# Optimization experiments

Hardware: AMD Instinct MI355X
Metric: run time of the kernel (lower is better)

## Reference

```python
import jax, jax.numpy as jnp
import numpy as np

N, E, D, ED, G = 50000, 800000, 64, 32, 50


def setup_inputs() -> dict:
    key = jax.random.key(0)
    ks = jax.random.split(key, 24)
    s = 0.05
    inp = {
        "x": jax.random.normal(ks[0], (N, D), jnp.float32),
        "edge_attr": jax.random.normal(ks[1], (E, ED), jnp.float32),
        "edge_index": jax.random.randint(ks[2], (2, E), 0, N, jnp.int64),
    }
    i = 3
    for step in range(2):
        inp[f"fe{step}_W1"] = jax.random.normal(ks[i], (2 * D + ED, D), jnp.float32) * s; i += 1
        inp[f"fe{step}_b1"] = jnp.zeros((D,), jnp.float32)
        inp[f"fe{step}_W2"] = jax.random.normal(ks[i], (D, D), jnp.float32) * s; i += 1
        inp[f"fe{step}_b2"] = jnp.zeros((D,), jnp.float32)
        inp[f"lstm{step}_Wih"] = jax.random.normal(ks[i], (D, 4 * D), jnp.float32) * s; i += 1
        inp[f"lstm{step}_Whh"] = jax.random.normal(ks[i], (D, 4 * D), jnp.float32) * s; i += 1
        inp[f"lstm{step}_bih"] = jnp.zeros((4 * D,), jnp.float32)
        inp[f"lstm{step}_bhh"] = jnp.zeros((4 * D,), jnp.float32)
    inp["gm_W"] = jax.random.normal(ks[i], (D, G), jnp.float32) * s; i += 1
    inp["gm_b"] = jnp.zeros((G,), jnp.float32)
    inp["fm_W"] = jax.random.normal(ks[i], (D, G), jnp.float32) * s; i += 1
    inp["fm_b"] = jnp.zeros((G,), jnp.float32)
    return inp


def _mpn(x, edge_attr, src, dst, W1, b1, W2, b2):
    # x_i = x[dst] (target), x_j = x[src] (source); aggregate 'add' at dst
    m = jnp.concatenate([x[dst], x[src], edge_attr], axis=1)  # [E, 2D+ED]
    m = jax.nn.relu(m @ W1 + b1) @ W2 + b2                    # [E, D]
    return jax.ops.segment_sum(m, dst, num_segments=x.shape[0])


def _lstm_cell(inp, h, c, Wih, Whh, bih, bhh):
    gates = inp @ Wih + h @ Whh + (bih + bhh)  # [N, 4D], gate order i,f,g,o
    i, f, g, o = jnp.split(gates, 4, axis=1)
    c = jax.nn.sigmoid(f) * c + jax.nn.sigmoid(i) * jnp.tanh(g)
    h = jax.nn.sigmoid(o) * jnp.tanh(c)
    return h, c


def reference(x, edge_attr, edge_index,
              fe0_W1, fe0_b1, fe0_W2, fe0_b2,
              lstm0_Wih, lstm0_Whh, lstm0_bih, lstm0_bhh,
              fe1_W1, fe1_b1, fe1_W2, fe1_b2,
              lstm1_Wih, lstm1_Whh, lstm1_bih, lstm1_bhh,
              gm_W, gm_b, fm_W, fm_b):
    src, dst = edge_index[0], edge_index[1]
    c = jnp.zeros_like(x)
    fes = [(fe0_W1, fe0_b1, fe0_W2, fe0_b2), (fe1_W1, fe1_b1, fe1_W2, fe1_b2)]
    lstms = [(lstm0_Wih, lstm0_Whh, lstm0_bih, lstm0_bhh),
             (lstm1_Wih, lstm1_Whh, lstm1_bih, lstm1_bhh)]
    for step in range(2):
        a = _mpn(x, edge_attr, src, dst, *fes[step])
        # LSTMCell(input=x, (h=a, c=c)) as in the original forward
        x, c = _lstm_cell(x, a, c, *lstms[step])
    g = jax.nn.sigmoid(x @ gm_W + gm_b)   # [N, G]
    h_v_G = x @ fm_W + fm_b               # [N, G]
    return jnp.sum(g * h_v_G, axis=0)     # [G]
```

## Files before the change

### kernel.cpp

```cpp
#include <hip/hip_runtime.h>
#include <hip/hip_bf16.h>

using short8 = __attribute__((ext_vector_type(8))) short;
using f32x4  = __attribute__((ext_vector_type(4))) float;

#define KLP 136

__device__ __forceinline__ unsigned short f2bf(float f) {
  unsigned u = __float_as_uint(f);
  u += 0x7FFFu + ((u >> 16) & 1u);
  return (unsigned short)(u >> 16);
}
__device__ __forceinline__ unsigned pack2(float a, float b) {
  return (unsigned)f2bf(a) | ((unsigned)f2bf(b) << 16);
}
#if __has_builtin(__builtin_amdgcn_rcpf)
__device__ __forceinline__ float fast_rcp(float x) { return __builtin_amdgcn_rcpf(x); }
#else
__device__ __forceinline__ float fast_rcp(float x) { return 1.f / x; }
#endif
__device__ __forceinline__ float sigm(float x) { return fast_rcp(1.f + __expf(-x)); }
__device__ __forceinline__ float tanh_f(float x) { return fmaf(2.f, sigm(2.f * x), -1.f); }

__global__ __launch_bounds__(256) void prep_all(
    const float* __restrict__ x,
    const float* __restrict__ W1_0, const float* __restrict__ Wih0,
    const float* __restrict__ bih0, const float* __restrict__ bhh0,
    const float* __restrict__ W1_1, const float* __restrict__ Wih1,
    const float* __restrict__ bih1, const float* __restrict__ bhh1,
    const float* __restrict__ W2_0, const float* __restrict__ Whh0, const float* __restrict__ b2_0,
    const float* __restrict__ W2_1, const float* __restrict__ Whh1, const float* __restrict__ b2_1,
    const float* __restrict__ gmW, const float* __restrict__ fmW,
    unsigned short* __restrict__ W1T,
    unsigned short* __restrict__ WcT,
    float* __restrict__ bG,
    float* __restrict__ b2h,
    unsigned short* __restrict__ WrT,
    unsigned short* __restrict__ xb0,
    float* __restrict__ aggrH,
    int* __restrict__ histA,
    float* __restrict__ outZ, int nOut,
    int N)
{
  int t = blockIdx.x * 256 + threadIdx.x;

  const int R0 = 2 * 26880 + 8192;
  if (t < R0) {
    const int per = 26880;
    if (t >= 2 * per) {
      int r2 = t - 2 * per;
      int o = r2 >> 6, k = r2 & 63;
      float v = 0.f;
      if (o < 50) v = gmW[k * 50 + o];
      else if (o >= 64 && o < 114) v = fmW[k * 50 + (o - 64)];
      WrT[o * 64 + k] = f2bf(v);
      return;
    }
    int step = t / per, r = t % per;
    const float* W1  = step ? W1_1 : W1_0;
    const float* Wih = step ? Wih1 : Wih0;
    const float* bih = step ? bih1 : bih0;
    const float* bhh = step ? bhh1 : bhh0;
    if (r < 10240) {
      int o = r / 160, k = r % 160;
      W1T[step * 10240 + o * 160 + k] = f2bf(W1[k * 64 + o]);
    } else if (r < 26624) {
      int rr = r - 10240;
      int g = rr >> 6, k = rr & 63;
      WcT[step * 32768 + g * 128 + k] = f2bf(Wih[k * 256 + g]);
    } else {
      int g = r - 26624;
      bG[step * 256 + g] = bih[g] + bhh[g];
    }
    return;
  }
  t -= R0;

  const int R1 = 33280;
  if (t < R1) {
    if (t < 32768) {
      int step = t >> 14, r = t & 16383;
      int g = r >> 6, k = r & 63;
      const float* W2  = step ? W2_1 : W2_0;
      const float* Whh = step ? Whh1 : Whh0;
      float v = 0.f;
      for (int j = 0; j < 64; ++j) v = fmaf(W2[k * 64 + j], Whh[j * 256 + g], v);
      WcT[step * 32768 + g * 128 + 64 + k] = f2bf(v);
    } else {
      int r = t - 32768;
      int step = r >> 8, g = r & 255;
      const float* b2  = step ? b2_1 : b2_0;
      const float* Whh = step ? Whh1 : Whh0;
      float v = 0.f;
      for (int j = 0; j < 64; ++j) v = fmaf(b2[j], Whh[j * 256 + g], v);
      b2h[step * 256 + g] = v;
    }
    return;
  }
  t -= R1;

  const int R2 = N * 8;
  if (t < R2) {
    const float4* p = (const float4*)(x + (long long)t * 8);
    float4 a0 = p[0], a1 = p[1];
    *(uint4*)(xb0 + (long long)t * 8) =
        make_uint4(pack2(a0.x, a0.y), pack2(a0.z, a0.w), pack2(a1.x, a1.y), pack2(a1.z, a1.w));
    return;
  }
  t -= R2;

  const int R3 = N * 16;
  if (t < R3) { ((float4*)aggrH)[t] = make_float4(0.f, 0.f, 0.f, 0.f); return; }
  t -= R3;

  const int R4 = N / 4;
  if (t < R4) { ((int4*)histA)[t] = make_int4(0, 0, 0, 0); return; }
  t -= R4;

  if (t < nOut) outZ[t] = 0.f;
}

__global__ __launch_bounds__(256) void hist_kernel(
    const int* __restrict__ dstI, int* __restrict__ hist, int E)
{
  int e = blockIdx.x * 256 + threadIdx.x;
  if (e < E) atomicAdd(&hist[dstI[e]], 1);
}

__global__ __launch_bounds__(256) void scan_part(
    const int* __restrict__ hist, int2* __restrict__ blockTot, int N)
{
  __shared__ int sD[256], sS[256];
  int t = threadIdx.x;
  int n = blockIdx.x * 256 + t;
  int d = (n < N) ? hist[n] : 0;
  int sg = (d + 15) >> 4;
  sD[t] = d; sS[t] = sg;
  __syncthreads();
  #pragma unroll
  for (int off = 128; off; off >>= 1) {
    if (t < off) { sD[t] += sD[t + off]; sS[t] += sS[t + off]; }
    __syncthreads();
  }
  if (t == 0) blockTot[blockIdx.x] = make_int2(sD[0], sS[0]);
}

__global__ __launch_bounds__(256) void scan_mid(
    const int2* __restrict__ blockTot, int2* __restrict__ blockBase,
    int* __restrict__ nSegTot, int nb)
{
  __shared__ int sD[256], sS[256];
  int t = threadIdx.x;
  int d = 0, s = 0;
  if (t < nb) { int2 v = blockTot[t]; d = v.x; s = v.y; }
  sD[t] = d; sS[t] = s;
  __syncthreads();
  #pragma unroll
  for (int off = 1; off < 256; off <<= 1) {
    int vd = (t >= off) ? sD[t - off] : 0;
    int vs = (t >= off) ? sS[t - off] : 0;
    __syncthreads();
    sD[t] += vd; sS[t] += vs;
    __syncthreads();
  }
  if (t < nb) blockBase[t] = make_int2(sD[t] - d, sS[t] - s);
  if (t == nb - 1) *nSegTot = sS[t];
}

__global__ __launch_bounds__(256) void scan_final(
    const int* __restrict__ hist, const int2* __restrict__ blockBase,
    int* __restrict__ cursor, int4* __restrict__ segInfo, int N)
{
  __shared__ int sD[256], sS[256];
  int t = threadIdx.x;
  int n = blockIdx.x * 256 + t;
  int d = (n < N) ? hist[n] : 0;
  int sg = (d + 15) >> 4;
  sD[t] = d; sS[t] = sg;
  __syncthreads();
  #pragma unroll
  for (int off = 1; off < 256; off <<= 1) {
    int vd = (t >= off) ? sD[t - off] : 0;
    int vs = (t >= off) ? sS[t - off] : 0;
    __syncthreads();
    sD[t] += vd; sS[t] += vs;
    __syncthreads();
  }
  if (n < N) {
    int2 bb = blockBase[blockIdx.x];
    int degBase = bb.x + sD[t] - d;
    int segBase = bb.y + sS[t] - sg;
    cursor[n] = degBase;
    for (int j = 0; j < sg; ++j)
      segInfo[segBase + j] = make_int4(degBase + j * 16, n, min(d - j * 16, 16), 0);
  }
}

__global__ __launch_bounds__(256) void scatter_perm(
    const int* __restrict__ srcI, const int* __restrict__ dstI,
    const float* __restrict__ ea, int* __restrict__ cursor,
    int* __restrict__ srcS, unsigned short* __restrict__ eaS, int E)
{
  const int t = threadIdx.x;
  const int l = t & 63;
  const int e = blockIdx.x * 64 + (t >> 2);
  const int c = t & 3;
  if (e >= E) return;
  int p = 0;
  if (c == 0) {
    int d = dstI[e];
    p = atomicAdd(&cursor[d], 1);
    srcS[p] = srcI[e];
  }
  p = __shfl(p, l & ~3);
  const float4* pe = (const float4*)(ea + (long long)e * 32 + c * 8);
  float4 a0 = pe[0], a1 = pe[1];
  *(uint4*)(eaS + (long long)p * 32 + c * 8) =
      make_uint4(pack2(a0.x, a0.y), pack2(a0.z, a0.w), pack2(a1.x, a1.y), pack2(a1.z, a1.w));
}

__global__ __launch_bounds__(256) void dst_gemm(
    const unsigned short* __restrict__ xb,
    const unsigned short* __restrict__ W1T,
    const float* __restrict__ b1,
    float* __restrict__ D,
    int nNodes)
{
  __shared__ unsigned short sX[64 * 72];
  const int t = threadIdx.x;
  const int base = blockIdx.x * 64;
  const int nl = t >> 2, q = t & 3;
  const int node = base + nl;
  {
    uint4* dst = (uint4*)(sX + nl * 72 + q * 16);
    if (node < nNodes) {
      const uint4* px = (const uint4*)(xb + (long long)node * 64);
      dst[0] = px[q * 2];
      dst[1] = px[q * 2 + 1];
    } else {
      dst[0] = make_uint4(0, 0, 0, 0);
      dst[1] = make_uint4(0, 0, 0, 0);
    }
  }
  const int w = t >> 6, l = t & 63, quad = l >> 4, lr = l & 15;
  short8 bF[2][4];
  #pragma unroll
  for (int kc = 0; kc < 2; ++kc)
    #pragma unroll
    for (int n = 0; n < 4; ++n)
      bF[kc][n] = *(const short8*)(W1T + (n * 16 + lr) * 160 + kc * 32 + quad * 8);
  float bb[4];
  #pragma unroll
  for (int n = 0; n < 4; ++n) bb[n] = b1[n * 16 + lr];
  __syncthreads();

  f32x4 acc[4] = {};
  #pragma unroll
  for (int kc = 0; kc < 2; ++kc) {
    short8 aF = *(const short8*)(sX + (w * 16 + lr) * 72 + kc * 32 + quad * 8);
    #pragma unroll
    for (int n = 0; n < 4; ++n)
      acc[n] = __builtin_amdgcn_mfma_f32_16x16x32_bf16(aF, bF[kc][n], acc[n], 0, 0, 0);
  }
  #pragma unroll
  for (int n = 0; n < 4; ++n) {
    #pragma unroll
    for (int rr = 0; rr < 4; ++rr) {
      int nd = base + w * 16 + quad * 4 + rr;
      if (nd < nNodes)
        D[(long long)nd * 64 + n * 16 + lr] = acc[n][rr] + bb[n];
    }
  }
}

__global__ __launch_bounds__(256) void edge_gemm(
    const unsigned short* __restrict__ xb,
    const unsigned short* __restrict__ eaS,
    const int* __restrict__ srcS,
    const int4* __restrict__ segInfo,
    const int* __restrict__ nSegPtr,
    const unsigned short* __restrict__ W1T,
    const float* __restrict__ D,
    float* __restrict__ aggrH)
{
  __shared__ unsigned short stash[12 * 64 * 8];
  const int t = threadIdx.x;
  const int w = t >> 6, l = t & 63;
  const int quad = l >> 4, lr = l & 15;

  #pragma unroll
  for (int p = 0; p < 3; ++p) {
    int idx = p * 256 + t;
    int grp = idx >> 6, ll = idx & 63;
    int kc = 2 + (grp >> 2), n = grp & 3;
    *(uint4*)(stash + idx * 8) =
        *(const uint4*)(W1T + (n * 16 + (ll & 15)) * 160 + kc * 32 + (ll >> 4) * 8);
  }
  __syncthreads();

  const int nSeg = *nSegPtr;
  const int W = gridDim.x * 4;
  int s = blockIdx.x * 4 + w;
  if (s >= nSeg) return;

  int4 si = segInfo[s];
  short8 A2, A3, A4;
  float Dv0, Dv1, Dv2, Dv3;
  {
    int src0 = srcS[si.x + min(lr, si.z - 1)];
    const short8* ps = (const short8*)(xb + (long long)src0 * 64);
    A2 = ps[quad];
    A3 = ps[4 + quad];
    A4 = *(const short8*)(eaS + (long long)(si.x + min(lr, si.z - 1)) * 32 + quad * 8);
    const float* dp = D + (long long)si.y * 64 + lr;
    Dv0 = dp[0]; Dv1 = dp[16]; Dv2 = dp[32]; Dv3 = dp[48];
  }
  int sn = s + W;
  bool more = sn < nSeg;
  int4 si_n = si;
  int src_n = 0;
  if (more) {
    si_n = segInfo[sn];
    src_n = srcS[si_n.x + min(lr, si_n.z - 1)];
  }

  while (true) {
    short8 B2 = A2, B3 = A3, B4 = A4;
    float En0 = Dv0, En1 = Dv1, En2 = Dv2, En3 = Dv3;
    if (more) {
      const short8* ps = (const short8*)(xb + (long long)src_n * 64);
      B2 = ps[quad];
      B3 = ps[4 + quad];
      B4 = *(const short8*)(eaS + (long long)(si_n.x + min(lr, si_n.z - 1)) * 32 + quad * 8);
      const float* dp = D + (long long)si_n.y * 64 + lr;
      En0 = dp[0]; En1 = dp[16]; En2 = dp[32]; En3 = dp[48];
    }
    int snn = sn + W;
    bool more2 = more && (snn < nSeg);
    int4 si_nn = si_n;
    int src_nn = src_n;
    if (more2) {
      si_nn = segInfo[snn];
      src_nn = srcS[si_nn.x + min(lr, si_nn.z - 1)];
    }

    const int node = si.y, cnt = si.z;
    f32x4 acc[4] = {};
    #pragma unroll
    for (int kc = 0; kc < 3; ++kc) {
      short8 aX = (kc == 0) ? A2 : (kc == 1) ? A3 : A4;
      #pragma unroll
      for (int n = 0; n < 4; ++n) {
        short8 bFr = *(const short8*)(stash + (((kc << 2) | n) * 64 + l) * 8);
        acc[n] = __builtin_amdgcn_mfma_f32_16x16x32_bf16(aX, bFr, acc[n], 0, 0, 0);
      }
    }

    float myv = 0.f;
    #pragma unroll
    for (int n = 0; n < 4; ++n) {
      float bias = (n == 0) ? Dv0 : (n == 1) ? Dv1 : (n == 2) ? Dv2 : Dv3;
      float sum = 0.f;
      #pragma unroll
      for (int rr = 0; rr < 4; ++rr) {
        float v = fmaxf(acc[n][rr] + bias, 0.f);
        sum += (quad * 4 + rr < cnt) ? v : 0.f;
      }
      sum += __shfl_xor(sum, 16);
      sum += __shfl_xor(sum, 32);
      if (quad == n) myv = sum;
    }
    unsafeAtomicAdd(&aggrH[(long long)node * 64 + l], myv);

    if (!more) break;
    si = si_n; A2 = B2; A3 = B3; A4 = B4;
    Dv0 = En0; Dv1 = En1; Dv2 = En2; Dv3 = En3;
    sn = snn; si_n = si_nn; src_n = src_nn; more = more2;
  }
}

__global__ __launch_bounds__(256) void lstm3(
    const unsigned short* __restrict__ xbin,
    float* __restrict__ aggrH,
    const float* __restrict__ cin,
    float* __restrict__ cout,
    const unsigned short* __restrict__ WcT,
    const float* __restrict__ bG,
    const float* __restrict__ b2h,
    const int* __restrict__ degA,
    unsigned short* __restrict__ xbout,
    const unsigned short* __restrict__ WrT,
    const float* __restrict__ gb, const float* __restrict__ fb,
    float* __restrict__ outG,
    int nNodes, int zeroAggr, int doReadout)
{
  __shared__ unsigned short sIn[64 * KLP];
  __shared__ unsigned short sW[128 * 72];
  __shared__ float sBG[256], sB2h[256];
  const int t = threadIdx.x;
  sBG[t] = bG[t];
  sB2h[t] = b2h[t];

  const int base_n = blockIdx.x * 64;
  const int nl = t >> 2, q = t & 3;
  const int node = base_n + nl;
  unsigned short* rowp = sIn + nl * KLP;
  if (node < nNodes) {
    const uint4* px = (const uint4*)(xbin + (long long)node * 64);
    *(uint4*)(rowp + q * 16)     = px[q * 2];
    *(uint4*)(rowp + q * 16 + 8) = px[q * 2 + 1];
    float4* pg = (float4*)(aggrH + (long long)node * 64) + q * 4;
    float4 g0 = pg[0], g1 = pg[1], g2 = pg[2], g3 = pg[3];
    *(uint4*)(rowp + 64 + q * 16) =
        make_uint4(pack2(g0.x, g0.y), pack2(g0.z, g0.w), pack2(g1.x, g1.y), pack2(g1.z, g1.w));
    *(uint4*)(rowp + 64 + q * 16 + 8) =
        make_uint4(pack2(g2.x, g2.y), pack2(g2.z, g2.w), pack2(g3.x, g3.y), pack2(g3.z, g3.w));
    if (zeroAggr) {
      float4 z = make_float4(0.f, 0.f, 0.f, 0.f);
      pg[0] = z; pg[1] = z; pg[2] = z; pg[3] = z;
    }
  } else {
    *(uint4*)(rowp + q * 16)          = make_uint4(0, 0, 0, 0);
    *(uint4*)(rowp + q * 16 + 8)      = make_uint4(0, 0, 0, 0);
    *(uint4*)(rowp + 64 + q * 16)     = make_uint4(0, 0, 0, 0);
    *(uint4*)(rowp + 64 + q * 16 + 8) = make_uint4(0, 0, 0, 0);
  }

  const int w = t >> 6, l = t & 63, quad = l >> 4, lr = l & 15;
  const int row0 = w * 16;
  f32x4 acc[16] = {};
  for (int grp = 0; grp < 4; ++grp) {
    const uint4* gw = (const uint4*)WcT + (long long)(grp * 64) * 16;
    uint4* lw = (uint4*)sW;
    {
      int o0 = t >> 4, s4 = t & 15;
      #pragma unroll
      for (int pp = 0; pp < 4; ++pp) {
        int o = pp * 16 + o0;
        lw[o * 17 + s4] = gw[o * 16 + s4];
      }
    }
    __syncthreads();
    #pragma unroll
    for (int kc = 0; kc < 4; ++kc) {
      short8 aF = *(const short8*)(sIn + (row0 + lr) * KLP + kc * 32 + quad * 8);
      #pragma unroll
      for (int nt = 0; nt < 4; ++nt) {
        short8 bF = *(const short8*)(sW + (nt * 16 + lr) * KLP + kc * 32 + quad * 8);
        acc[grp * 4 + nt] = __builtin_amdgcn_mfma_f32_16x16x32_bf16(aF, bF, acc[grp * 4 + nt], 0, 0, 0);
      }
    }
    __syncthreads();
  }

  #pragma unroll
  for (int nt = 0; nt < 4; ++nt) {
    #pragma unroll
    for (int rr = 0; rr < 4; ++rr) {
      int node2 = base_n + row0 + quad * 4 + rr;
      int rl = row0 + quad * 4 + rr;
      int col = nt * 16 + lr;
      if (node2 < nNodes) {
        long long off = (long long)node2 * 64 + col;
        float dg = (float)degA[node2];
        float iv = acc[nt][rr]      + sBG[col]       + dg * sB2h[col];
        float fv = acc[4 + nt][rr]  + sBG[64 + col]  + dg * sB2h[64 + col];
        float gv = acc[8 + nt][rr]  + sBG[128 + col] + dg * sB2h[128 + col];
        float ov = acc[12 + nt][rr] + sBG[192 + col] + dg * sB2h[192 + col];
        float cOld = cin ? cin[off] : 0.f;
        float cN = sigm(fv) * cOld + sigm(iv) * tanh_f(gv);
        float hN = sigm(ov) * tanh_f(cN);
        if (doReadout) {
          sIn[rl * 72 + col] = f2bf(hN);
        } else {
          cout[off] = cN;
          xbout[off] = f2bf(hN);
        }
      } else if (doReadout) {
        sIn[rl * 72 + col] = 0;
      }
    }
  }

  if (!doReadout) return;

  __syncthreads();
  {
    const uint4* gw = (const uint4*)WrT;
    uint4* lw = (uint4*)sW;
    #pragma unroll
    for (int pp = 0; pp < 4; ++pp) {
      int idx = t + pp * 256;
      int o = idx >> 3, s = idx & 7;
      lw[o * 9 + s] = gw[idx];
    }
  }
  if (t < 64) {
    sBG[t]      = (t < 50) ? gb[t] : 0.f;
    sBG[64 + t] = (t < 50) ? fb[t] : 0.f;
  }
  __syncthreads();

  f32x4 racc[8] = {};
  #pragma unroll
  for (int kc = 0; kc < 2; ++kc) {
    short8 aF = *(const short8*)(sIn + (w * 16 + lr) * 72 + kc * 32 + quad * 8);
    #pragma unroll
    for (int n = 0; n < 8; ++n) {
      short8 bF = *(const short8*)(sW + (n * 16 + lr) * 72 + kc * 32 + quad * 8);
      racc[n] = __builtin_amdgcn_mfma_f32_16x16x32_bf16(aF, bF, racc[n], 0, 0, 0);
    }
  }
  float* sOutF = sB2h;
  #pragma unroll
  for (int n = 0; n < 4; ++n) {
    float val = 0.f;
    #pragma unroll
    for (int rr = 0; rr < 4; ++rr) {
      int nd = base_n + w * 16 + quad * 4 + rr;
      if (nd < nNodes) {
        int jj = n * 16 + lr;
        float gv = sigm(racc[n][rr] + sBG[jj]);
        float fv = racc[n + 4][rr] + sBG[64 + jj];
        val += gv * fv;
      }
    }
    val += __shfl_xor(val, 16);
    val += __shfl_xor(val, 32);
    if (quad == 0) sOutF[w * 64 + n * 16 + lr] = val;
  }
  __syncthreads();
  if (t < 50) {
    float sm = sOutF[t] + sOutF[64 + t] + sOutF[128 + t] + sOutF[192 + t];
    unsafeAtomicAdd(&outG[t], sm);
  }
}

extern "C" void kernel_launch(void* const* d_in, const int* in_sizes, int n_in,
                              void* d_out, int out_size, void* d_ws, size_t ws_size,
                              hipStream_t stream)
{
  const float* x      = (const float*)d_in[0];
  const float* ea     = (const float*)d_in[1];
  const int*   ei     = (const int*)d_in[2];
  const float* fe0_W1 = (const float*)d_in[3];
  const float* fe0_b1 = (const float*)d_in[4];
  const float* fe0_W2 = (const float*)d_in[5];
  const float* fe0_b2 = (const float*)d_in[6];
  const float* l0_Wih = (const float*)d_in[7];
  const float* l0_Whh = (const float*)d_in[8];
  const float* l0_bih = (const float*)d_in[9];
  const float* l0_bhh = (const float*)d_in[10];
  const float* fe1_W1 = (const float*)d_in[11];
  const float* fe1_b1 = (const float*)d_in[12];
  const float* fe1_W2 = (const float*)d_in[13];
  const float* fe1_b2 = (const float*)d_in[14];
  const float* l1_Wih = (const float*)d_in[15];
  const float* l1_Whh = (const float*)d_in[16];
  const float* l1_bih = (const float*)d_in[17];
  const float* l1_bhh = (const float*)d_in[18];
  const float* gm_W   = (const float*)d_in[19];
  const float* gm_b   = (const float*)d_in[20];
  const float* fm_W   = (const float*)d_in[21];
  const float* fm_b   = (const float*)d_in[22];

  const int N = in_sizes[0] / 64;
  const int E = in_sizes[1] / 32;
  const int* srcI = ei;
  const int* dstI = ei + E;

  char* ws = (char*)d_ws;
  unsigned short* xb0     = (unsigned short*)(ws + 0);
  unsigned short* xb1     = (unsigned short*)(ws + 6400000);
  float*          aggrH   = (float*)(ws + 12800000);
  float*          cbuf    = (float*)(ws + 25600000);
  unsigned short* eaS     = (unsigned short*)(ws + 38400000);
  int*            srcS    = (int*)(ws + 89601024);
  int4*           segInfo = (int4*)(ws + 92801088);
  int*            histA   = (int*)(ws + 94401280);
  int*            curA    = (int*)(ws + 94601280);
  unsigned short* W1T     = (unsigned short*)(ws + 94801280);
  unsigned short* WcT     = (unsigned short*)(ws + 94842240);
  float*          bG      = (float*)(ws + 94973312);
  float*          b2h     = (float*)(ws + 94975360);
  unsigned short* WrT     = (unsigned short*)(ws + 94977408);
  int*            nSegPtr = (int*)(ws + 94993792);
  int2*           blockTot  = (int2*)(ws + 94993856);
  int2*           blockBase = (int2*)(ws + 94995904);
  float*          Dbuf    = (float*)(ws + 96000000);

  const int prepT = (2 * 26880 + 8192) + 33280 + N * 8 + N * 16 + N / 4 + out_size;
  prep_all<<<(prepT + 255) / 256, 256, 0, stream>>>(
      x,
      fe0_W1, l0_Wih, l0_bih, l0_bhh,
      fe1_W1, l1_Wih, l1_bih, l1_bhh,
      fe0_W2, l0_Whh, fe0_b2,
      fe1_W2, l1_Whh, fe1_b2,
      gm_W, fm_W,
      W1T, WcT, bG, b2h, WrT, xb0,
      aggrH, histA, (float*)d_out, out_size, N);

  const int nb = (N + 255) / 256;
  hist_kernel<<<(E + 255) / 256, 256, 0, stream>>>(dstI, histA, E);
  scan_part<<<nb, 256, 0, stream>>>(histA, blockTot, N);
  scan_mid<<<1, 256, 0, stream>>>(blockTot, blockBase, nSegPtr, nb);
  scan_final<<<nb, 256, 0, stream>>>(histA, blockBase, curA, segInfo, N);
  scatter_perm<<<(E + 63) / 64, 256, 0, stream>>>(srcI, dstI, ea, curA, srcS, eaS, E);

  const int nodeBlocks = (N + 63) / 64;

  dst_gemm<<<nodeBlocks, 256, 0, stream>>>(xb0, W1T, fe0_b1, Dbuf, N);
  edge_gemm<<<2048, 256, 0, stream>>>(xb0, eaS, srcS, segInfo, nSegPtr,
                                      W1T, Dbuf, aggrH);
  lstm3<<<nodeBlocks, 256, 0, stream>>>(xb0, aggrH, nullptr, cbuf, WcT, bG, b2h,
                                        histA, xb1, WrT, gm_b, fm_b, (float*)d_out,
                                        N, 1, 0);

  dst_gemm<<<nodeBlocks, 256, 0, stream>>>(xb1, W1T + 10240, fe1_b1, Dbuf, N);
  edge_gemm<<<2048, 256, 0, stream>>>(xb1, eaS, srcS, segInfo, nSegPtr,
                                      W1T + 10240, Dbuf, aggrH);
  lstm3<<<nodeBlocks, 256, 0, stream>>>(xb1, aggrH, cbuf, nullptr, WcT + 32768,
                                        bG + 256, b2h + 256, histA, nullptr,
                                        WrT, gm_b, fm_b, (float*)d_out,
                                        N, 0, 1);
}
```

Measured before the change: 423.9 us.

## Fuse step-1 dst GEMM into LSTM and give edge_gemm contiguous segment ranges

The first LSTM kernel now also computes the next message-passing step's destination-projection term (h @ W1 dst slice + b1) from the staged hidden state in LDS. This removes a separate dst_gemm launch and its re-read of xb1. Separately, edge_gemm warps now process a contiguous chunk of segments rather than a grid-strided set. Consecutive segments of the same node are summed in registers and flushed with a single atomic, which cuts global atomics. Contiguous chunking can unbalance work across warps and shortens the prefetch distance from two segments to one.

```diff
diff --git a/kernel.cpp b/kernel.cpp
--- a/kernel.cpp
+++ b/kernel.cpp
@@ -299,49 +299,42 @@
   __syncthreads();
 
   const int nSeg = *nSegPtr;
-  const int W = gridDim.x * 4;
-  int s = blockIdx.x * 4 + w;
-  if (s >= nSeg) return;
+  const int TW = gridDim.x * 4;
+  const int C = (nSeg + TW - 1) / TW;
+  int s = (blockIdx.x * 4 + w) * C;
+  const int sEnd = min(s + C, nSeg);
+  if (s >= sEnd) return;
 
   int4 si = segInfo[s];
   short8 A2, A3, A4;
   float Dv0, Dv1, Dv2, Dv3;
   {
-    int src0 = srcS[si.x + min(lr, si.z - 1)];
+    int pos = si.x + min(lr, si.z - 1);
+    int src0 = srcS[pos];
     const short8* ps = (const short8*)(xb + (long long)src0 * 64);
     A2 = ps[quad];
     A3 = ps[4 + quad];
-    A4 = *(const short8*)(eaS + (long long)(si.x + min(lr, si.z - 1)) * 32 + quad * 8);
+    A4 = *(const short8*)(eaS + (long long)pos * 32 + quad * 8);
     const float* dp = D + (long long)si.y * 64 + lr;
     Dv0 = dp[0]; Dv1 = dp[16]; Dv2 = dp[32]; Dv3 = dp[48];
   }
-  int sn = s + W;
-  bool more = sn < nSeg;
-  int4 si_n = si;
-  int src_n = 0;
-  if (more) {
-    si_n = segInfo[sn];
-    src_n = srcS[si_n.x + min(lr, si_n.z - 1)];
-  }
+  float carry = 0.f;
 
   while (true) {
+    const bool more = (s + 1) < sEnd;
+    int4 si_n = si;
     short8 B2 = A2, B3 = A3, B4 = A4;
     float En0 = Dv0, En1 = Dv1, En2 = Dv2, En3 = Dv3;
     if (more) {
+      si_n = segInfo[s + 1];
+      int pos_n = si_n.x + min(lr, si_n.z - 1);
+      int src_n = srcS[pos_n];
       const short8* ps = (const short8*)(xb + (long long)src_n * 64);
       B2 = ps[quad];
       B3 = ps[4 + quad];
-      B4 = *(const short8*)(eaS + (long long)(si_n.x + min(lr, si_n.z - 1)) * 32 + quad * 8);
+      B4 = *(const short8*)(eaS + (long long)pos_n * 32 + quad * 8);
       const float* dp = D + (long long)si_n.y * 64 + lr;
       En0 = dp[0]; En1 = dp[16]; En2 = dp[32]; En3 = dp[48];
-    }
-    int snn = sn + W;
-    bool more2 = more && (snn < nSeg);
-    int4 si_nn = si_n;
-    int src_nn = src_n;
-    if (more2) {
-      si_nn = segInfo[snn];
-      src_nn = srcS[si_nn.x + min(lr, si_nn.z - 1)];
     }
 
     const int node = si.y, cnt = si.z;
@@ -370,12 +363,16 @@
       sum += __shfl_xor(sum, 32);
       if (quad == n) myv = sum;
     }
-    unsafeAtomicAdd(&aggrH[(long long)node * 64 + l], myv);
-
+    carry += myv;
+
+    if (!more || si_n.y != node) {
+      unsafeAtomicAdd(&aggrH[(long long)node * 64 + l], carry);
+      carry = 0.f;
+    }
     if (!more) break;
+    ++s;
     si = si_n; A2 = B2; A3 = B3; A4 = B4;
     Dv0 = En0; Dv1 = En1; Dv2 = En2; Dv3 = En3;
-    sn = snn; si_n = si_nn; src_n = src_nn; more = more2;
   }
 }
 
@@ -392,7 +389,10 @@
     const unsigned short* __restrict__ WrT,
     const float* __restrict__ gb, const float* __restrict__ fb,
     float* __restrict__ outG,
-    int nNodes, int zeroAggr, int doReadout)
+    const unsigned short* __restrict__ W1n,
+    const float* __restrict__ b1n,
+    float* __restrict__ Dout,
+    int nNodes, int zeroAggr, int doReadout, int doD)
 {
   __shared__ unsigned short sIn[64 * KLP];
   __shared__ unsigned short sW[128 * 72];
@@ -453,6 +453,7 @@
     __syncthreads();
   }
 
+  const int stageH = doReadout | doD;
   #pragma unroll
   for (int nt = 0; nt < 4; ++nt) {
     #pragma unroll
@@ -470,14 +471,44 @@
         float cOld = cin ? cin[off] : 0.f;
         float cN = sigm(fv) * cOld + sigm(iv) * tanh_f(gv);
         float hN = sigm(ov) * tanh_f(cN);
-        if (doReadout) {
-          sIn[rl * 72 + col] = f2bf(hN);
-        } else {
+        unsigned short hb = f2bf(hN);
+        if (stageH) sIn[rl * 72 + col] = hb;
+        if (!doReadout) {
           cout[off] = cN;
-          xbout[off] = f2bf(hN);
+          xbout[off] = hb;
         }
-      } else if (doReadout) {
+      } else if (stageH) {
         sIn[rl * 72 + col] = 0;
+      }
+    }
+  }
+
+  if (doD) {
+    __syncthreads();
+    short8 bFn[2][4];
+    #pragma unroll
+    for (int kc = 0; kc < 2; ++kc)
+      #pragma unroll
+      for (int n = 0; n < 4; ++n)
+        bFn[kc][n] = *(const short8*)(W1n + (n * 16 + lr) * 160 + kc * 32 + quad * 8);
+    float bbn[4];
+    #pragma unroll
+    for (int n = 0; n < 4; ++n) bbn[n] = b1n[n * 16 + lr];
+    f32x4 acc2[4] = {};
+    #pragma unroll
+    for (int kc = 0; kc < 2; ++kc) {
+      short8 aF = *(const short8*)(sIn + (w * 16 + lr) * 72 + kc * 32 + quad * 8);
+      #pragma unroll
+      for (int n = 0; n < 4; ++n)
+        acc2[n] = __builtin_amdgcn_mfma_f32_16x16x32_bf16(aF, bFn[kc][n], acc2[n], 0, 0, 0);
+    }
+    #pragma unroll
+    for (int n = 0; n < 4; ++n) {
+      #pragma unroll
+      for (int rr = 0; rr < 4; ++rr) {
+        int nd = base_n + w * 16 + quad * 4 + rr;
+        if (nd < nNodes)
+          Dout[(long long)nd * 64 + n * 16 + lr] = acc2[n][rr] + bbn[n];
       }
     }
   }
@@ -614,13 +645,14 @@
                                       W1T, Dbuf, aggrH);
   lstm3<<<nodeBlocks, 256, 0, stream>>>(xb0, aggrH, nullptr, cbuf, WcT, bG, b2h,
                                         histA, xb1, WrT, gm_b, fm_b, (float*)d_out,
-                                        N, 1, 0);
-
-  dst_gemm<<<nodeBlocks, 256, 0, stream>>>(xb1, W1T + 10240, fe1_b1, Dbuf, N);
+                                        W1T + 10240, fe1_b1, Dbuf,
+                                        N, 1, 0, 1);
+
   edge_gemm<<<2048, 256, 0, stream>>>(xb1, eaS, srcS, segInfo, nSegPtr,
                                       W1T + 10240, Dbuf, aggrH);
   lstm3<<<nodeBlocks, 256, 0, stream>>>(xb1, aggrH, cbuf, nullptr, WcT + 32768,
                                         bG + 256, b2h + 256, histA, nullptr,
                                         WrT, gm_b, fm_b, (float*)d_out,
-                                        N, 0, 1);
-}
+                                        W1T, fe0_b1, Dbuf,
+                                        N, 0, 1, 0);
+}
```

New measurement: 434.5 us. 2.5% more time.
